# Kernel optimization log

Hardware: AMD Instinct MI355X
Metric: run time of the kernel (lower is better)

## Reference

```python
import jax, jax.numpy as jnp
import numpy as np

EMBED = 1024
MLP = 2048
N_EXPERTS = 8
TOP_K = 2


def setup_inputs() -> dict:
    key = jax.random.key(0)
    ks = jax.random.split(key, 5)
    scale_e = 1.0 / np.sqrt(EMBED)
    scale_m = 1.0 / np.sqrt(MLP)
    x = jax.random.normal(ks[0], (4, 2048, EMBED), dtype=jnp.float32)
    gate_w = jax.random.normal(ks[1], (EMBED, N_EXPERTS), dtype=jnp.float32) * scale_e
    w1 = jax.random.normal(ks[2], (N_EXPERTS, EMBED, MLP), dtype=jnp.float32) * scale_e
    w3 = jax.random.normal(ks[3], (N_EXPERTS, EMBED, MLP), dtype=jnp.float32) * scale_e
    w2 = jax.random.normal(ks[4], (N_EXPERTS, MLP, EMBED), dtype=jnp.float32) * scale_m
    return {"x": x, "gate_w": gate_w, "w1": w1, "w2": w2, "w3": w3}


def reference(x, gate_w, w1, w2, w3):
    B, S, D = x.shape
    xf = x.reshape(-1, D)  # [T, D] tokens
    # Router: softmax over experts, top-k select, renormalize selected weights
    router_logits = xf @ gate_w                      # [T, E]
    routing_weights = jax.nn.softmax(router_logits, axis=-1)
    sel_w, sel_e = jax.lax.top_k(routing_weights, TOP_K)  # [T, K]
    sel_w = sel_w / jnp.sum(sel_w, axis=-1, keepdims=True)
    out = jnp.zeros_like(xf)
    # Loop over the small fixed expert set; tokens not routed to expert e get
    # coefficient 0, matching the gather/scatter-add combine of the original.
    for e in range(N_EXPERTS):
        coef = jnp.sum(jnp.where(sel_e == e, sel_w, 0.0), axis=-1)  # [T]
        h = jax.nn.silu(xf @ w1[e]) * (xf @ w3[e])                  # [T, Mlp] SwiGLU
        out = out + coef[:, None] * (h @ w2[e])                     # [T, D]
    return out.reshape(B, S, D)
```

## Files before the change

kernel.cpp:

```cpp
#include <hip/hip_runtime.h>

#define EMBED 1024
#define MLP   2048
#define NE    8
#define NTOK  8192
#define RMAX  (2*NTOK + NE*256)

typedef _Float16 f16x8 __attribute__((ext_vector_type(8)));
typedef _Float16 f16x4 __attribute__((ext_vector_type(4)));
typedef float    f32x4 __attribute__((ext_vector_type(4)));

__device__ __forceinline__ void async_copy16(const void* g, void* l) {
  __builtin_amdgcn_global_load_lds(
      (const __attribute__((address_space(1))) unsigned int*)g,
      (__attribute__((address_space(3))) unsigned int*)l, 16, 0, 0);
}

__global__ __launch_bounds__(256) void router_kernel(
    const float* __restrict__ x, const float* __restrict__ gw,
    int* __restrict__ sel_e, float* __restrict__ sel_w, int* __restrict__ counts)
{
  __shared__ float gwt[NE * EMBED];
  __shared__ int cnt[NE];
  int tid = threadIdx.x;
  for (int idx = tid; idx < NE * EMBED; idx += 256) {
    int i = idx >> 3, e = idx & 7;
    gwt[e * EMBED + i] = gw[idx];
  }
  if (tid < NE) cnt[tid] = 0;
  __syncthreads();

  int lane = tid & 63, wv = tid >> 6;
  int t = blockIdx.x * 4 + wv;
  const float4* xr = (const float4*)(x + (size_t)t * EMBED);
  const float4* gt4 = (const float4*)gwt;
  float acc[NE];
  #pragma unroll
  for (int e = 0; e < NE; ++e) acc[e] = 0.f;
  #pragma unroll
  for (int c = 0; c < 4; ++c) {
    float4 xv = xr[c * 64 + lane];
    #pragma unroll
    for (int e = 0; e < NE; ++e) {
      float4 gv = gt4[e * 256 + c * 64 + lane];
      acc[e] += xv.x * gv.x + xv.y * gv.y + xv.z * gv.z + xv.w * gv.w;
    }
  }
  #pragma unroll
  for (int off = 1; off < 64; off <<= 1) {
    #pragma unroll
    for (int e = 0; e < NE; ++e) acc[e] += __shfl_xor(acc[e], off);
  }
  if (lane == 0) {
    int e0 = 0; float l0 = acc[0];
    #pragma unroll
    for (int e = 1; e < NE; ++e) if (acc[e] > l0) { l0 = acc[e]; e0 = e; }
    int e1 = -1; float l1 = -1e30f;
    #pragma unroll
    for (int e = 0; e < NE; ++e) if (e != e0 && acc[e] > l1) { l1 = acc[e]; e1 = e; }
    float w0 = 1.f / (1.f + expf(l1 - l0));
    sel_e[2 * t] = e0;     sel_w[2 * t] = w0;
    sel_e[2 * t + 1] = e1; sel_w[2 * t + 1] = 1.f - w0;
    atomicAdd(&cnt[e0], 1); atomicAdd(&cnt[e1], 1);
  }
  __syncthreads();
  if (tid < NE && cnt[tid]) atomicAdd(&counts[tid], cnt[tid]);
}

__global__ __launch_bounds__(256) void assign_kernel(
    const int* __restrict__ sel_e, const float* __restrict__ sel_w,
    const int* __restrict__ counts, int* __restrict__ cursor,
    int* __restrict__ offs_out, int* __restrict__ rowtok,
    float* __restrict__ rowcoef, int* __restrict__ inv)
{
  int offl[NE];
  {
    int o = 0;
    #pragma unroll
    for (int e = 0; e < NE; ++e) { offl[e] = o; o += (counts[e] + 255) & ~255; }
    if (blockIdx.x == 0 && threadIdx.x == 0) {
      #pragma unroll
      for (int e = 0; e < NE; ++e) offs_out[e] = offl[e];
      offs_out[NE] = o;
    }
  }
  int t = blockIdx.x * 256 + threadIdx.x;
  int lane = threadIdx.x & 63;
  #pragma unroll
  for (int k = 0; k < 2; ++k) {
    int e = sel_e[2 * t + k];
    float w = sel_w[2 * t + k];
    for (int xch = 0; xch < NE; ++xch) {
      unsigned long long m = __ballot(e == xch);
      if (e == xch) {
        int leader = __ffsll((unsigned long long)m) - 1;
        int base = 0;
        if (lane == leader) base = atomicAdd(&cursor[xch], (int)__popcll(m));
        base = __shfl(base, leader);
        int pos = offl[xch] + base + (int)__popcll(m & ((1ull << lane) - 1));
        rowtok[pos] = t;
        rowcoef[pos] = w;
        inv[2 * t + k] = pos;
      }
    }
  }
}

__global__ __launch_bounds__(256) void gather_kernel(
    const float* __restrict__ x, const int* __restrict__ rowtok,
    _Float16* __restrict__ xg)
{
  int r = blockIdx.x;
  int tok = rowtok[r];
  int t4 = threadIdx.x * 4;
  _Float16* dst = xg + (size_t)r * EMBED + t4;
  if (tok >= 0) {
    float4 v = *(const float4*)(x + (size_t)tok * EMBED + t4);
    f16x4 h; h.x = (_Float16)v.x; h.y = (_Float16)v.y; h.z = (_Float16)v.z; h.w = (_Float16)v.w;
    *(f16x4*)dst = h;
  } else {
    f16x4 z = {(_Float16)0.f, (_Float16)0.f, (_Float16)0.f, (_Float16)0.f};
    *(f16x4*)dst = z;
  }
}

__global__ __launch_bounds__(256) void transpose_all_kernel(
    const float* __restrict__ w1, const float* __restrict__ w3,
    const float* __restrict__ w2, _Float16* __restrict__ w1t,
    _Float16* __restrict__ w3t, _Float16* __restrict__ w2t)
{
  int id = blockIdx.x;
  int mat = id >> 12;
  int rr = id & 4095;
  int e = rr >> 9, tile = rr & 511;
  const float* src; _Float16* dst; int K, N;
  if (mat == 0)      { src = w1; dst = w1t; K = EMBED; N = MLP; }
  else if (mat == 1) { src = w3; dst = w3t; K = EMBED; N = MLP; }
  else               { src = w2; dst = w2t; K = MLP;   N = EMBED; }
  int nx = K >> 6;
  int k0 = (tile % nx) * 64, n0 = (tile / nx) * 64;
  src += (size_t)e * K * N;
  dst += (size_t)e * K * N;

  __shared__ float tilebuf[64][65];
  int t = threadIdx.x;
  int r = t >> 4, c4 = (t & 15) * 4;
  #pragma unroll
  for (int i = 0; i < 4; ++i) {
    float4 v = *(const float4*)(src + (size_t)(k0 + r + 16 * i) * N + n0 + c4);
    tilebuf[r + 16 * i][c4 + 0] = v.x;
    tilebuf[r + 16 * i][c4 + 1] = v.y;
    tilebuf[r + 16 * i][c4 + 2] = v.z;
    tilebuf[r + 16 * i][c4 + 3] = v.w;
  }
  __syncthreads();
  int kk8 = (t & 7) * 8, nIdx = t >> 3;
  #pragma unroll
  for (int i = 0; i < 2; ++i) {
    int n = nIdx + 32 * i;
    f16x8 h;
    #pragma unroll
    for (int j = 0; j < 8; ++j) h[j] = (_Float16)tilebuf[kk8 + j][n];
    *(f16x8*)(dst + (size_t)(n0 + n) * K + k0 + kk8) = h;
  }
}

__device__ __forceinline__ int resolve_expert(const int* __restrict__ offs, int r0)
{
  int e = 0;
  #pragma unroll
  for (int q = 0; q < NE - 1; ++q) if (r0 >= offs[q + 1]) e = q + 1;
  return e;
}

__device__ __forceinline__ const _Float16* frag_addr(const _Float16* buf, int row, int quad)
{
  return buf + row * 32 + ((quad ^ ((row >> 1) & 3)) << 3);
}

__device__ __forceinline__ void swz_block(int& x, int& y)
{
  int lin = blockIdx.y * 144 + blockIdx.x;
  int xcd = lin & 7, idx = lin >> 3;
  x = xcd * 18 + idx % 18;
  y = idx / 18;
}

__global__ __launch_bounds__(256, 2) void gemm1_kernel(
    const _Float16* __restrict__ xg, const _Float16* __restrict__ w1t,
    const _Float16* __restrict__ w3t, const float* __restrict__ rowcoef,
    const int* __restrict__ offs, _Float16* __restrict__ hb)
{
  int bx, by; swz_block(bx, by);
  int r0 = bx * 128;
  if (r0 >= offs[NE]) return;
  int e = resolve_expert(offs, r0);
  int n0 = by * 128;
  const _Float16* B1 = w1t + (size_t)e * MLP * EMBED;
  const _Float16* B3 = w3t + (size_t)e * MLP * EMBED;

  __shared__ __align__(16) _Float16 As[3][128 * 32];
  __shared__ __align__(16) _Float16 Bs1[3][128 * 32];
  __shared__ __align__(16) _Float16 Bs3[3][128 * 32];

  int tid = threadIdx.x, lane = tid & 63, wv = tid >> 6;
  int wm = (wv & 1) << 6, wn = (wv >> 1) << 6;
  int l16 = lane & 15, quad = lane >> 4;

  int row0 = tid >> 2, kqp = tid & 3;
  int row1 = row0 + 64;
  int kql0 = kqp ^ ((row0 >> 1) & 3);
  int kql1 = kqp ^ ((row1 >> 1) & 3);
  size_t gA0 = (size_t)(r0 + row0) * EMBED + kql0 * 8;
  size_t gA1 = (size_t)(r0 + row1) * EMBED + kql1 * 8;
  size_t gB0 = (size_t)(n0 + row0) * EMBED + kql0 * 8;
  size_t gB1 = (size_t)(n0 + row1) * EMBED + kql1 * 8;
  int lof0 = (wv * 64) * 8;
  int lof1 = (256 + wv * 64) * 8;

  f32x4 acc1[4][4], acc3[4][4];
  f32x4 z4 = {0.f, 0.f, 0.f, 0.f};
  #pragma unroll
  for (int i = 0; i < 4; ++i)
    #pragma unroll
    for (int j = 0; j < 4; ++j) { acc1[i][j] = z4; acc3[i][j] = z4; }

  auto stage = [&](int b, int kk) {
    async_copy16(xg + gA0 + kk, &As[b][lof0]);
    async_copy16(xg + gA1 + kk, &As[b][lof1]);
    async_copy16(B1 + gB0 + kk, &Bs1[b][lof0]);
    async_copy16(B1 + gB1 + kk, &Bs1[b][lof1]);
    async_copy16(B3 + gB0 + kk, &Bs3[b][lof0]);
    async_copy16(B3 + gB1 + kk, &Bs3[b][lof1]);
  };

  const int NIT = EMBED / 32;
  stage(0, 0);
  for (int k = 0; k < NIT; ++k) {
    int b = k % 3;
    if (k + 1 < NIT) {
      stage((k + 1) % 3, (k + 1) * 32);
      asm volatile("s_waitcnt vmcnt(6)" ::: "memory");
    } else {
      asm volatile("s_waitcnt vmcnt(0)" ::: "memory");
    }
    asm volatile("s_barrier" ::: "memory");

    f16x8 af[4], b1f[4], b3f[4];
    #pragma unroll
    for (int i = 0; i < 4; ++i)
      af[i] = *(const f16x8*)frag_addr(As[b], wm + 16 * i + l16, quad);
    #pragma unroll
    for (int j = 0; j < 4; ++j) {
      b1f[j] = *(const f16x8*)frag_addr(Bs1[b], wn + 16 * j + l16, quad);
      b3f[j] = *(const f16x8*)frag_addr(Bs3[b], wn + 16 * j + l16, quad);
    }
    #pragma unroll
    for (int i = 0; i < 4; ++i)
      #pragma unroll
      for (int j = 0; j < 4; ++j) {
        acc1[i][j] = __builtin_amdgcn_mfma_f32_16x16x32_f16(af[i], b1f[j], acc1[i][j], 0, 0, 0);
        acc3[i][j] = __builtin_amdgcn_mfma_f32_16x16x32_f16(af[i], b3f[j], acc3[i][j], 0, 0, 0);
      }
  }

  #pragma unroll
  for (int i = 0; i < 4; ++i) {
    int mb = r0 + wm + 16 * i + quad * 4;
    float cf[4];
    #pragma unroll
    for (int rg = 0; rg < 4; ++rg) cf[rg] = rowcoef[mb + rg];
    #pragma unroll
    for (int j = 0; j < 4; ++j) {
      int col = n0 + wn + 16 * j + l16;
      #pragma unroll
      for (int rg = 0; rg < 4; ++rg) {
        float g = acc1[i][j][rg], u = acc3[i][j][rg];
        float h = g * u * cf[rg] / (1.f + __expf(-g));
        hb[(size_t)(mb + rg) * MLP + col] = (_Float16)h;
      }
    }
  }
}

__global__ __launch_bounds__(256, 2) void gemm2_kernel(
    const _Float16* __restrict__ hb, const _Float16* __restrict__ w2t,
    const int* __restrict__ offs, _Float16* __restrict__ hb2)
{
  int bx, by; swz_block(bx, by);
  int r0 = bx * 128;
  if (r0 >= offs[NE]) return;
  int e = resolve_expert(offs, r0);
  int n0 = by * 128;
  const _Float16* B = w2t + (size_t)e * EMBED * MLP;

  __shared__ __align__(16) _Float16 As[3][128 * 32];
  __shared__ __align__(16) _Float16 Bs[3][128 * 32];

  int tid = threadIdx.x, lane = tid & 63, wv = tid >> 6;
  int wm = (wv & 1) << 6, wn = (wv >> 1) << 6;
  int l16 = lane & 15, quad = lane >> 4;

  int row0 = tid >> 2, kqp = tid & 3;
  int row1 = row0 + 64;
  int kql0 = kqp ^ ((row0 >> 1) & 3);
  int kql1 = kqp ^ ((row1 >> 1) & 3);
  size_t gA0 = (size_t)(r0 + row0) * MLP + kql0 * 8;
  size_t gA1 = (size_t)(r0 + row1) * MLP + kql1 * 8;
  size_t gB0 = (size_t)(n0 + row0) * MLP + kql0 * 8;
  size_t gB1 = (size_t)(n0 + row1) * MLP + kql1 * 8;
  int lof0 = (wv * 64) * 8;
  int lof1 = (256 + wv * 64) * 8;

  f32x4 acc[4][4];
  f32x4 z4 = {0.f, 0.f, 0.f, 0.f};
  #pragma unroll
  for (int i = 0; i < 4; ++i)
    #pragma unroll
    for (int j = 0; j < 4; ++j) acc[i][j] = z4;

  auto stage = [&](int b, int kk) {
    async_copy16(hb + gA0 + kk, &As[b][lof0]);
    async_copy16(hb + gA1 + kk, &As[b][lof1]);
    async_copy16(B  + gB0 + kk, &Bs[b][lof0]);
    async_copy16(B  + gB1 + kk, &Bs[b][lof1]);
  };

  const int NIT = MLP / 32;
  stage(0, 0);
  for (int k = 0; k < NIT; ++k) {
    int b = k % 3;
    if (k + 1 < NIT) {
      stage((k + 1) % 3, (k + 1) * 32);
      asm volatile("s_waitcnt vmcnt(4)" ::: "memory");
    } else {
      asm volatile("s_waitcnt vmcnt(0)" ::: "memory");
    }
    asm volatile("s_barrier" ::: "memory");

    f16x8 af[4], bf[4];
    #pragma unroll
    for (int i = 0; i < 4; ++i)
      af[i] = *(const f16x8*)frag_addr(As[b], wm + 16 * i + l16, quad);
    #pragma unroll
    for (int j = 0; j < 4; ++j)
      bf[j] = *(const f16x8*)frag_addr(Bs[b], wn + 16 * j + l16, quad);
    #pragma unroll
    for (int i = 0; i < 4; ++i)
      #pragma unroll
      for (int j = 0; j < 4; ++j)
        acc[i][j] = __builtin_amdgcn_mfma_f32_16x16x32_f16(af[i], bf[j], acc[i][j], 0, 0, 0);
  }

  #pragma unroll
  for (int i = 0; i < 4; ++i) {
    int mb = r0 + wm + 16 * i + quad * 4;
    #pragma unroll
    for (int j = 0; j < 4; ++j) {
      int col = n0 + wn + 16 * j + l16;
      #pragma unroll
      for (int rg = 0; rg < 4; ++rg)
        hb2[(size_t)(mb + rg) * EMBED + col] = (_Float16)acc[i][j][rg];
    }
  }
}

__global__ __launch_bounds__(256) void combine_kernel(
    const _Float16* __restrict__ hb2, const int* __restrict__ inv,
    float* __restrict__ out)
{
  int t = blockIdx.x;
  int d = threadIdx.x * 4;
  int p0 = inv[2 * t], p1 = inv[2 * t + 1];
  f16x4 a = *(const f16x4*)(hb2 + (size_t)p0 * EMBED + d);
  f16x4 b = *(const f16x4*)(hb2 + (size_t)p1 * EMBED + d);
  float4 r;
  r.x = (float)a.x + (float)b.x;
  r.y = (float)a.y + (float)b.y;
  r.z = (float)a.z + (float)b.z;
  r.w = (float)a.w + (float)b.w;
  *(float4*)(out + (size_t)t * EMBED + d) = r;
}

extern "C" void kernel_launch(void* const* d_in, const int* in_sizes, int n_in,
                              void* d_out, int out_size, void* d_ws, size_t ws_size,
                              hipStream_t stream)
{
  (void)in_sizes; (void)n_in; (void)ws_size; (void)out_size;
  const float* x  = (const float*)d_in[0];
  const float* gw = (const float*)d_in[1];
  const float* w1 = (const float*)d_in[2];
  const float* w2 = (const float*)d_in[3];
  const float* w3 = (const float*)d_in[4];
  float* out = (float*)d_out;
  char* ws = (char*)d_ws;

  size_t o = 0;
  auto alloc = [&](size_t bytes) { size_t r = o; o = (o + bytes + 255) & ~255ULL; return r; };
  const size_t wbytes = (size_t)NE * MLP * EMBED * 2;
  _Float16* w1t = (_Float16*)(ws + alloc(wbytes));
  _Float16* w3t = (_Float16*)(ws + alloc(wbytes));
  _Float16* w2t = (_Float16*)(ws + alloc(wbytes));
  _Float16* xg  = (_Float16*)(ws + alloc((size_t)RMAX * EMBED * 2));
  _Float16* hb  = (_Float16*)(ws + alloc((size_t)RMAX * MLP * 2));
  int*   rowtok  = (int*)(ws + alloc((size_t)RMAX * 4));
  float* rowcoef = (float*)(ws + alloc((size_t)RMAX * 4));
  int*   sel_e   = (int*)(ws + alloc((size_t)2 * NTOK * 4));
  float* sel_w   = (float*)(ws + alloc((size_t)2 * NTOK * 4));
  int*   inv     = (int*)(ws + alloc((size_t)2 * NTOK * 4));
  int*   meta    = (int*)(ws + alloc(256));
  int* counts = meta;
  int* offs   = meta + 8;
  int* cursor = meta + 17;
  _Float16* hb2 = xg;

  hipMemsetAsync(meta, 0, 256, stream);
  hipMemsetAsync(rowtok, 0xFF, (size_t)RMAX * 4, stream);
  hipMemsetAsync(rowcoef, 0, (size_t)RMAX * 4, stream);

  transpose_all_kernel<<<3 * 4096, 256, 0, stream>>>(w1, w3, w2, w1t, w3t, w2t);

  router_kernel<<<NTOK / 4, 256, 0, stream>>>(x, gw, sel_e, sel_w, counts);
  assign_kernel<<<NTOK / 256, 256, 0, stream>>>(sel_e, sel_w, counts, cursor,
                                                offs, rowtok, rowcoef, inv);
  gather_kernel<<<RMAX, 256, 0, stream>>>(x, rowtok, xg);

  gemm1_kernel<<<dim3(RMAX / 128, MLP / 128), 256, 0, stream>>>(xg, w1t, w3t, rowcoef, offs, hb);
  gemm2_kernel<<<dim3(RMAX / 128, EMBED / 128), 256, 0, stream>>>(hb, w2t, offs, hb2);
  combine_kernel<<<NTOK, 256, 0, stream>>>(hb2, inv, out);
}
```

Baseline: 594.5 us.

## Interleave w1/w3 into one fused weight and deepen GEMM pipelines to four stages

```diff
diff --git a/kernel.cpp b/kernel.cpp
--- a/kernel.cpp
+++ b/kernel.cpp
@@ -2,6 +2,7 @@
 
 #define EMBED 1024
 #define MLP   2048
+#define MLP2  4096
 #define NE    8
 #define NTOK  8192
 #define RMAX  (2*NTOK + NE*256)
@@ -126,21 +127,21 @@
 
 __global__ __launch_bounds__(256) void transpose_all_kernel(
     const float* __restrict__ w1, const float* __restrict__ w3,
-    const float* __restrict__ w2, _Float16* __restrict__ w1t,
-    _Float16* __restrict__ w3t, _Float16* __restrict__ w2t)
+    const float* __restrict__ w2, _Float16* __restrict__ w13t,
+    _Float16* __restrict__ w2t)
 {
   int id = blockIdx.x;
   int mat = id >> 12;
   int rr = id & 4095;
   int e = rr >> 9, tile = rr & 511;
-  const float* src; _Float16* dst; int K, N;
-  if (mat == 0)      { src = w1; dst = w1t; K = EMBED; N = MLP; }
-  else if (mat == 1) { src = w3; dst = w3t; K = EMBED; N = MLP; }
-  else               { src = w2; dst = w2t; K = MLP;   N = EMBED; }
+  const float* src; _Float16* dst; int K, N; size_t estride;
+  if (mat == 0)      { src = w1; dst = w13t; K = EMBED; N = MLP; estride = (size_t)MLP2 * EMBED; }
+  else if (mat == 1) { src = w3; dst = w13t; K = EMBED; N = MLP; estride = (size_t)MLP2 * EMBED; }
+  else               { src = w2; dst = w2t;  K = MLP;   N = EMBED; estride = (size_t)MLP * EMBED; }
   int nx = K >> 6;
   int k0 = (tile % nx) * 64, n0 = (tile / nx) * 64;
   src += (size_t)e * K * N;
-  dst += (size_t)e * K * N;
+  dst += (size_t)e * estride;
 
   __shared__ float tilebuf[64][65];
   int t = threadIdx.x;
@@ -161,7 +162,11 @@
     f16x8 h;
     #pragma unroll
     for (int j = 0; j < 8; ++j) h[j] = (_Float16)tilebuf[kk8 + j][n];
-    *(f16x8*)(dst + (size_t)(n0 + n) * K + k0 + kk8) = h;
+    int nn = n0 + n;
+    size_t drow;
+    if (mat == 2) drow = nn;
+    else          drow = 2 * (nn & ~15) + (nn & 15) + (mat == 1 ? 16 : 0);
+    *(f16x8*)(dst + drow * K + k0 + kk8) = h;
   }
 }
 
@@ -187,21 +192,19 @@
 }
 
 __global__ __launch_bounds__(256, 2) void gemm1_kernel(
-    const _Float16* __restrict__ xg, const _Float16* __restrict__ w1t,
-    const _Float16* __restrict__ w3t, const float* __restrict__ rowcoef,
-    const int* __restrict__ offs, _Float16* __restrict__ hb)
+    const _Float16* __restrict__ xg, const _Float16* __restrict__ w13t,
+    const float* __restrict__ rowcoef, const int* __restrict__ offs,
+    _Float16* __restrict__ hb)
 {
   int bx, by; swz_block(bx, by);
   int r0 = bx * 128;
   if (r0 >= offs[NE]) return;
   int e = resolve_expert(offs, r0);
   int n0 = by * 128;
-  const _Float16* B1 = w1t + (size_t)e * MLP * EMBED;
-  const _Float16* B3 = w3t + (size_t)e * MLP * EMBED;
-
-  __shared__ __align__(16) _Float16 As[3][128 * 32];
-  __shared__ __align__(16) _Float16 Bs1[3][128 * 32];
-  __shared__ __align__(16) _Float16 Bs3[3][128 * 32];
+  const _Float16* B = w13t + (size_t)e * MLP2 * EMBED;
+
+  __shared__ __align__(16) _Float16 As[4][128 * 32];
+  __shared__ __align__(16) _Float16 Bs[4][128 * 32];
 
   int tid = threadIdx.x, lane = tid & 63, wv = tid >> 6;
   int wm = (wv & 1) << 6, wn = (wv >> 1) << 6;
@@ -218,52 +221,50 @@
   int lof0 = (wv * 64) * 8;
   int lof1 = (256 + wv * 64) * 8;
 
-  f32x4 acc1[4][4], acc3[4][4];
+  f32x4 acc[4][4];
   f32x4 z4 = {0.f, 0.f, 0.f, 0.f};
   #pragma unroll
   for (int i = 0; i < 4; ++i)
     #pragma unroll
-    for (int j = 0; j < 4; ++j) { acc1[i][j] = z4; acc3[i][j] = z4; }
+    for (int j = 0; j < 4; ++j) acc[i][j] = z4;
 
   auto stage = [&](int b, int kk) {
     async_copy16(xg + gA0 + kk, &As[b][lof0]);
     async_copy16(xg + gA1 + kk, &As[b][lof1]);
-    async_copy16(B1 + gB0 + kk, &Bs1[b][lof0]);
-    async_copy16(B1 + gB1 + kk, &Bs1[b][lof1]);
-    async_copy16(B3 + gB0 + kk, &Bs3[b][lof0]);
-    async_copy16(B3 + gB1 + kk, &Bs3[b][lof1]);
+    async_copy16(B + gB0 + kk, &Bs[b][lof0]);
+    async_copy16(B + gB1 + kk, &Bs[b][lof1]);
   };
 
   const int NIT = EMBED / 32;
   stage(0, 0);
+  stage(1, 32);
   for (int k = 0; k < NIT; ++k) {
-    int b = k % 3;
-    if (k + 1 < NIT) {
-      stage((k + 1) % 3, (k + 1) * 32);
-      asm volatile("s_waitcnt vmcnt(6)" ::: "memory");
+    int b = k & 3;
+    if (k + 2 < NIT) {
+      stage((k + 2) & 3, (k + 2) * 32);
+      asm volatile("s_waitcnt vmcnt(8)" ::: "memory");
+    } else if (k + 1 < NIT) {
+      asm volatile("s_waitcnt vmcnt(4)" ::: "memory");
     } else {
       asm volatile("s_waitcnt vmcnt(0)" ::: "memory");
     }
     asm volatile("s_barrier" ::: "memory");
 
-    f16x8 af[4], b1f[4], b3f[4];
+    f16x8 af[4], bf[4];
     #pragma unroll
     for (int i = 0; i < 4; ++i)
       af[i] = *(const f16x8*)frag_addr(As[b], wm + 16 * i + l16, quad);
     #pragma unroll
-    for (int j = 0; j < 4; ++j) {
-      b1f[j] = *(const f16x8*)frag_addr(Bs1[b], wn + 16 * j + l16, quad);
-      b3f[j] = *(const f16x8*)frag_addr(Bs3[b], wn + 16 * j + l16, quad);
-    }
+    for (int j = 0; j < 4; ++j)
+      bf[j] = *(const f16x8*)frag_addr(Bs[b], wn + 16 * j + l16, quad);
     #pragma unroll
     for (int i = 0; i < 4; ++i)
       #pragma unroll
-      for (int j = 0; j < 4; ++j) {
-        acc1[i][j] = __builtin_amdgcn_mfma_f32_16x16x32_f16(af[i], b1f[j], acc1[i][j], 0, 0, 0);
-        acc3[i][j] = __builtin_amdgcn_mfma_f32_16x16x32_f16(af[i], b3f[j], acc3[i][j], 0, 0, 0);
-      }
-  }
-
+      for (int j = 0; j < 4; ++j)
+        acc[i][j] = __builtin_amdgcn_mfma_f32_16x16x32_f16(af[i], bf[j], acc[i][j], 0, 0, 0);
+  }
+
+  int colbase = (((n0 + wn) >> 5) << 4) + l16;
   #pragma unroll
   for (int i = 0; i < 4; ++i) {
     int mb = r0 + wm + 16 * i + quad * 4;
@@ -271,11 +272,11 @@
     #pragma unroll
     for (int rg = 0; rg < 4; ++rg) cf[rg] = rowcoef[mb + rg];
     #pragma unroll
-    for (int j = 0; j < 4; ++j) {
-      int col = n0 + wn + 16 * j + l16;
+    for (int p = 0; p < 2; ++p) {
+      int col = colbase + 16 * p;
       #pragma unroll
       for (int rg = 0; rg < 4; ++rg) {
-        float g = acc1[i][j][rg], u = acc3[i][j][rg];
+        float g = acc[i][2 * p][rg], u = acc[i][2 * p + 1][rg];
         float h = g * u * cf[rg] / (1.f + __expf(-g));
         hb[(size_t)(mb + rg) * MLP + col] = (_Float16)h;
       }
@@ -294,8 +295,8 @@
   int n0 = by * 128;
   const _Float16* B = w2t + (size_t)e * EMBED * MLP;
 
-  __shared__ __align__(16) _Float16 As[3][128 * 32];
-  __shared__ __align__(16) _Float16 Bs[3][128 * 32];
+  __shared__ __align__(16) _Float16 As[4][128 * 32];
+  __shared__ __align__(16) _Float16 Bs[4][128 * 32];
 
   int tid = threadIdx.x, lane = tid & 63, wv = tid >> 6;
   int wm = (wv & 1) << 6, wn = (wv >> 1) << 6;
@@ -322,16 +323,19 @@
   auto stage = [&](int b, int kk) {
     async_copy16(hb + gA0 + kk, &As[b][lof0]);
     async_copy16(hb + gA1 + kk, &As[b][lof1]);
-    async_copy16(B  + gB0 + kk, &Bs[b][lof0]);
-    async_copy16(B  + gB1 + kk, &Bs[b][lof1]);
+    async_copy16(B + gB0 + kk, &Bs[b][lof0]);
+    async_copy16(B + gB1 + kk, &Bs[b][lof1]);
   };
 
   const int NIT = MLP / 32;
   stage(0, 0);
+  stage(1, 32);
   for (int k = 0; k < NIT; ++k) {
-    int b = k % 3;
-    if (k + 1 < NIT) {
-      stage((k + 1) % 3, (k + 1) * 32);
+    int b = k & 3;
+    if (k + 2 < NIT) {
+      stage((k + 2) & 3, (k + 2) * 32);
+      asm volatile("s_waitcnt vmcnt(8)" ::: "memory");
+    } else if (k + 1 < NIT) {
       asm volatile("s_waitcnt vmcnt(4)" ::: "memory");
     } else {
       asm volatile("s_waitcnt vmcnt(0)" ::: "memory");
@@ -397,12 +401,10 @@
 
   size_t o = 0;
   auto alloc = [&](size_t bytes) { size_t r = o; o = (o + bytes + 255) & ~255ULL; return r; };
-  const size_t wbytes = (size_t)NE * MLP * EMBED * 2;
-  _Float16* w1t = (_Float16*)(ws + alloc(wbytes));
-  _Float16* w3t = (_Float16*)(ws + alloc(wbytes));
-  _Float16* w2t = (_Float16*)(ws + alloc(wbytes));
-  _Float16* xg  = (_Float16*)(ws + alloc((size_t)RMAX * EMBED * 2));
-  _Float16* hb  = (_Float16*)(ws + alloc((size_t)RMAX * MLP * 2));
+  _Float16* w13t = (_Float16*)(ws + alloc((size_t)NE * MLP2 * EMBED * 2));
+  _Float16* w2t  = (_Float16*)(ws + alloc((size_t)NE * MLP * EMBED * 2));
+  _Float16* xg   = (_Float16*)(ws + alloc((size_t)RMAX * EMBED * 2));
+  _Float16* hb   = (_Float16*)(ws + alloc((size_t)RMAX * MLP * 2));
   int*   rowtok  = (int*)(ws + alloc((size_t)RMAX * 4));
   float* rowcoef = (float*)(ws + alloc((size_t)RMAX * 4));
   int*   sel_e   = (int*)(ws + alloc((size_t)2 * NTOK * 4));
@@ -418,14 +420,14 @@
   hipMemsetAsync(rowtok, 0xFF, (size_t)RMAX * 4, stream);
   hipMemsetAsync(rowcoef, 0, (size_t)RMAX * 4, stream);
 
-  transpose_all_kernel<<<3 * 4096, 256, 0, stream>>>(w1, w3, w2, w1t, w3t, w2t);
+  transpose_all_kernel<<<3 * 4096, 256, 0, stream>>>(w1, w3, w2, w13t, w2t);
 
   router_kernel<<<NTOK / 4, 256, 0, stream>>>(x, gw, sel_e, sel_w, counts);
   assign_kernel<<<NTOK / 256, 256, 0, stream>>>(sel_e, sel_w, counts, cursor,
                                                 offs, rowtok, rowcoef, inv);
   gather_kernel<<<RMAX, 256, 0, stream>>>(x, rowtok, xg);
 
-  gemm1_kernel<<<dim3(RMAX / 128, MLP / 128), 256, 0, stream>>>(xg, w1t, w3t, rowcoef, offs, hb);
+  gemm1_kernel<<<dim3(RMAX / 128, MLP2 / 128), 256, 0, stream>>>(xg, w13t, rowcoef, offs, hb);
   gemm2_kernel<<<dim3(RMAX / 128, EMBED / 128), 256, 0, stream>>>(hb, w2t, offs, hb2);
   combine_kernel<<<NTOK, 256, 0, stream>>>(hb2, inv, out);
 }
```

After: 659.3 us. +10.9%, slower.
